# Optimization experiments

Hardware: AMD Instinct MI355X
Metric: run time of the kernel (lower is better)

## Reference

```python
import jax, jax.numpy as jnp
import numpy as np

# Static config matching init_kwargs
T_Q, Q_H, Q_W = 8, 14, 14
T_K, K_H, K_W = 8, 14, 14


def _rel_idx(k_len, q_len):
    # ratios are round(max(ratio, 1.0)) per original code
    q_ratio = round(max(k_len / q_len, 1.0))
    k_ratio = round(max(q_len / k_len, 1.0))
    dist = jnp.arange(k_len)[:, None] * k_ratio - jnp.arange(q_len)[None, :] * q_ratio
    return dist + (q_len - 1) * q_ratio  # [k_len, q_len], values in [0, 2*max_dist]


def setup_inputs() -> dict:
    key = jax.random.key(0)
    k1, k2, k3, k4, k5 = jax.random.split(key, 5)
    B, N, C = 2, 8, 64
    return {
        "key": jax.random.normal(k1, (B, N, T_K, K_H, K_W, C), dtype=jnp.float32),
        "scores": jax.random.normal(k2, (B, N, T_Q * Q_H * Q_W, T_K * K_H * K_W), dtype=jnp.float32),
        "height_embeddings": jax.random.normal(k3, (2 * (max(Q_H, K_H) - 1) + 1, C), dtype=jnp.float32),
        "width_embeddings": jax.random.normal(k4, (2 * (max(Q_W, K_W) - 1) + 1, C), dtype=jnp.float32),
        "time_embeddings": jax.random.normal(k5, (2 * (max(T_Q, T_K) - 1) + 1, C), dtype=jnp.float32),
    }


def reference(key, scores, height_embeddings, width_embeddings, time_embeddings):
    B, N = key.shape[0], key.shape[1]
    # Gather relative-position embeddings: Rh [k_h, q_h, c], Rw [k_w, q_w, c], Rt [T_k, T_q, c]
    Rh = height_embeddings[_rel_idx(K_H, Q_H)]
    Rw = width_embeddings[_rel_idx(K_W, Q_W)]
    Rt = time_embeddings[_rel_idx(T_K, T_Q)]
    # key: [B, N, T_k, k_h, k_w, c]
    rel_h = jnp.einsum('hqc,bnshwc->bnqshw', Rh, key)  # q = q_h
    rel_w = jnp.einsum('wqc,bnshwc->bnqshw', Rw, key)  # q = q_w
    rel_t = jnp.einsum('sqc,bnshwc->bnqshw', Rt, key)  # q = T_q
    s = scores.reshape(B, N, T_Q, Q_H, Q_W, T_K, K_H, K_W)
    s = (s
         + rel_h[:, :, None, :, None, :, :, :]
         + rel_w[:, :, None, None, :, :, :, :]
         + rel_t[:, :, :, None, None, :, :, :])
    return s.reshape(B, N, T_Q * Q_H * Q_W, T_K * K_H * K_W)
```

## Files before the change

### kernel.cpp

```cpp
#include <hip/hip_runtime.h>


typedef float f4 __attribute__((ext_vector_type(4)));

#define BN_TOTAL    16
#define KLEN        1568
#define KLEN4       392
#define QLEN        1568
#define KV_TOTAL    (BN_TOTAL * KLEN)
#define REL_H_ELEMS (BN_TOTAL * 14 * KLEN)
#define REL_T_ELEMS (BN_TOTAL * 8 * KLEN)

#define EROWS  69
#define EPITCH 68

__global__ __launch_bounds__(256) void rel_fused(const float* __restrict__ key,
                                                 const float* __restrict__ hemb,
                                                 const float* __restrict__ wemb,
                                                 const float* __restrict__ temb,
                                                 float* __restrict__ relh,
                                                 float* __restrict__ relw,
                                                 float* __restrict__ relt)
{
    __shared__ float se[EROWS * EPITCH];
    for (int idx = threadIdx.x; idx < EROWS * 64; idx += 256) {
        int row = idx >> 6, c = idx & 63;
        float v;
        if (row < 27)      v = hemb[row * 64 + c];
        else if (row < 54) v = wemb[(row - 27) * 64 + c];
        else               v = temb[(row - 54) * 64 + c];
        se[row * EPITCH + c] = v;
    }
    __syncthreads();

    int tid  = threadIdx.x;
    int s    = tid & 3;
    int kv   = blockIdx.x * 64 + (tid >> 2);
    int bn   = kv / KLEN;
    int k    = kv - bn * KLEN;
    int tk   = k / 196;
    int khw  = k - tk * 196;
    int kh   = khw / 14;
    int kw   = khw - kh * 14;

    f4 kr[16];
    const f4* kp = (const f4*)key + (size_t)kv * 16;
#pragma unroll
    for (int c = 0; c < 16; ++c) kr[c] = kp[c];

#pragma unroll
    for (int j = 0; j < 9; ++j) {
        int qi = s + 4 * j;
        int row = (qi < 14) ? (kh - qi + 13)
                : (qi < 28) ? (kw - qi + 54)
                            : (tk - qi + 89);
        float* dst = (qi < 14) ? relh + (size_t)(bn * 14 + qi) * KLEN
                   : (qi < 28) ? relw + (size_t)(bn * 14 + qi - 14) * KLEN
                               : relt + (size_t)(bn * 8 + qi - 28) * KLEN;
        const f4* e = (const f4*)(se + row * EPITCH);
        f4 acc4 = {0.f, 0.f, 0.f, 0.f};
#pragma unroll
        for (int c = 0; c < 16; ++c) acc4 += kr[c] * e[c];
        dst[k] = acc4.x + acc4.y + acc4.z + acc4.w;
    }
}

#define CH4    56
#define NCH    7
#define SROWS  21
#define STAGE4 (SROWS * CH4)
#define TILE4  (98 * CH4)

__global__ __launch_bounds__(256) void add_staged(const f4* __restrict__ scores,
                                                  const f4* __restrict__ relh,
                                                  const f4* __restrict__ relw,
                                                  const f4* __restrict__ relt,
                                                  f4* __restrict__ out)
{
    __shared__ f4 se[STAGE4];

    int tid = threadIdx.x;
    int b   = blockIdx.x;
    int ch  = b % NCH;  b /= NCH;
    int half = b & 1;   b >>= 1;
    int tq  = b & 7;    b >>= 3;
    int bn  = b;
    int cbase = ch * CH4;

    const f4* wrow = relw + (size_t)(bn * 14) * KLEN4 + cbase;
    const f4* hrow = relh + (size_t)(bn * 14 + half * 7) * KLEN4 + cbase;
    const f4* trow = relt + (size_t)(bn * 8 + tq) * KLEN4 + cbase;

    for (int e = tid; e < STAGE4; e += 256) {
        int r = e / CH4, c = e - r * CH4;
        f4 v;
        if (r < 14) v = wrow[(size_t)r * KLEN4 + c];
        else        v = hrow[(size_t)(r - 14) * KLEN4 + c] + trow[c];
        se[e] = v;
    }

    int obase = (bn * QLEN + tq * 196 + half * 98) * KLEN4 + cbase;

#define EIDX(J, e, row, c, gi)                        \
    int e   = tid + (J) * 256;                        \
    int row = e / CH4;                                \
    int c   = e - row * CH4;                          \
    int gi  = obase + row * KLEN4 + c;

#define LOAD3(G, sv)                                  \
    {                                                 \
        _Pragma("unroll")                             \
        for (int jj = 0; jj < 3; ++jj) {              \
            EIDX(3 * (G) + jj, e, row, c, gi)         \
            sv[jj] = scores[gi];                      \
        }                                             \
    }

#define PROC3(G, sv)                                  \
    {                                                 \
        _Pragma("unroll")                             \
        for (int jj = 0; jj < 3; ++jj) {              \
            EIDX(3 * (G) + jj, e, row, c, gi)         \
            int qhl = row / 14, qw = row - qhl * 14;  \
            f4 v = sv[jj] + se[qw * CH4 + c]          \
                          + se[(14 + qhl) * CH4 + c]; \
            __builtin_nontemporal_store(v, out + gi); \
        }                                             \
    }

    f4 sA[3], sB[3];

    LOAD3(0, sA);
    LOAD3(1, sB);
    __syncthreads();

    PROC3(0, sA);  LOAD3(2, sA);
    PROC3(1, sB);  LOAD3(3, sB);
    PROC3(2, sA);  LOAD3(4, sA);
    PROC3(3, sB);  LOAD3(5, sB);
    PROC3(4, sA);  LOAD3(6, sA);
    PROC3(5, sB);
    PROC3(6, sA);

    if (tid < TILE4 - 21 * 256) {
        EIDX(21, e, row, c, gi)
        int qhl = row / 14, qw = row - qhl * 14;
        f4 v = scores[gi] + se[qw * CH4 + c] + se[(14 + qhl) * CH4 + c];
        __builtin_nontemporal_store(v, out + gi);
    }
#undef EIDX
#undef LOAD3
#undef PROC3
}

extern "C" void kernel_launch(void* const* d_in, const int* in_sizes, int n_in,
                              void* d_out, int out_size, void* d_ws, size_t ws_size,
                              hipStream_t stream)
{
    const float* key    = (const float*)d_in[0];
    const float* scores = (const float*)d_in[1];
    const float* hemb   = (const float*)d_in[2];
    const float* wemb   = (const float*)d_in[3];
    const float* temb   = (const float*)d_in[4];
    float*       out    = (float*)d_out;

    size_t need = (size_t)(REL_H_ELEMS * 2 + REL_T_ELEMS) * sizeof(float);
    if (ws_size < need) return;

    float* relh = (float*)d_ws;
    float* relw = relh + REL_H_ELEMS;
    float* relt = relw + REL_H_ELEMS;

    rel_fused<<<KV_TOTAL * 4 / 256, 256, 0, stream>>>(key, hemb, wemb, temb,
                                                      relh, relw, relt);

    add_staged<<<BN_TOTAL * 8 * 2 * NCH, 256, 0, stream>>>((const f4*)scores,
                                                           (const f4*)relh,
                                                           (const f4*)relw,
                                                           (const f4*)relt,
                                                           (f4*)out);
}
```

Measured before the change: 61.59 us.

## Deepen scores prefetch before staging and split rel kernel across more threads

In the add kernel, eight score vectors per thread are now prefetched into registers before the shared-memory staging of the relative-position rows, rather than six. The staging loads and the barrier therefore overlap with more outstanding global reads, and the remaining groups are software-pipelined across four register buffers. In the rel kernel, each key vector is now handled by 8 threads instead of 4, which doubles the grid and leaves each thread with at most 5 dot products instead of 9. The costs are higher register pressure in the add kernel and redundant key loads in the rel kernel.

Result: no change. 62.57 us (+1.6%).

```diff
diff --git a/kernel.cpp b/kernel.cpp
--- a/kernel.cpp
+++ b/kernel.cpp
@@ -34,8 +34,8 @@
     __syncthreads();
 
     int tid  = threadIdx.x;
-    int s    = tid & 3;
-    int kv   = blockIdx.x * 64 + (tid >> 2);
+    int s    = tid & 7;
+    int kv   = blockIdx.x * 32 + (tid >> 3);
     int bn   = kv / KLEN;
     int k    = kv - bn * KLEN;
     int tk   = k / 196;
@@ -49,19 +49,21 @@
     for (int c = 0; c < 16; ++c) kr[c] = kp[c];
 
 #pragma unroll
-    for (int j = 0; j < 9; ++j) {
-        int qi = s + 4 * j;
-        int row = (qi < 14) ? (kh - qi + 13)
-                : (qi < 28) ? (kw - qi + 54)
-                            : (tk - qi + 89);
-        float* dst = (qi < 14) ? relh + (size_t)(bn * 14 + qi) * KLEN
-                   : (qi < 28) ? relw + (size_t)(bn * 14 + qi - 14) * KLEN
-                               : relt + (size_t)(bn * 8 + qi - 28) * KLEN;
-        const f4* e = (const f4*)(se + row * EPITCH);
-        f4 acc4 = {0.f, 0.f, 0.f, 0.f};
+    for (int j = 0; j < 5; ++j) {
+        int qi = s + 8 * j;
+        if (qi < 36) {
+            int row = (qi < 14) ? (kh - qi + 13)
+                    : (qi < 28) ? (kw - qi + 54)
+                                : (tk - qi + 89);
+            float* dst = (qi < 14) ? relh + (size_t)(bn * 14 + qi) * KLEN
+                       : (qi < 28) ? relw + (size_t)(bn * 14 + qi - 14) * KLEN
+                                   : relt + (size_t)(bn * 8 + qi - 28) * KLEN;
+            const f4* e = (const f4*)(se + row * EPITCH);
+            f4 acc4 = {0.f, 0.f, 0.f, 0.f};
 #pragma unroll
-        for (int c = 0; c < 16; ++c) acc4 += kr[c] * e[c];
-        dst[k] = acc4.x + acc4.y + acc4.z + acc4.w;
+            for (int c = 0; c < 16; ++c) acc4 += kr[c] * e[c];
+            dst[k] = acc4.x + acc4.y + acc4.z + acc4.w;
+        }
     }
 }
 
@@ -87,70 +89,79 @@
     int bn  = b;
     int cbase = ch * CH4;
 
-    const f4* wrow = relw + (size_t)(bn * 14) * KLEN4 + cbase;
-    const f4* hrow = relh + (size_t)(bn * 14 + half * 7) * KLEN4 + cbase;
-    const f4* trow = relt + (size_t)(bn * 8 + tq) * KLEN4 + cbase;
+    int obase = (bn * QLEN + tq * 196 + half * 98) * KLEN4 + cbase;
 
-    for (int e = tid; e < STAGE4; e += 256) {
-        int r = e / CH4, c = e - r * CH4;
-        f4 v;
-        if (r < 14) v = wrow[(size_t)r * KLEN4 + c];
-        else        v = hrow[(size_t)(r - 14) * KLEN4 + c] + trow[c];
-        se[e] = v;
+#define MKIDX(E, row, c, gi)                          \
+    int row = (E) / CH4;                              \
+    int c   = (E) - row * CH4;                        \
+    int gi  = obase + row * KLEN4 + c;
+
+#define LOADG(G, sv)                                              \
+    {                                                             \
+        int eA = (G) * 512 + tid;                                 \
+        MKIDX(eA, rA, cA, giA)                                    \
+        sv[0] = scores[giA];                                      \
+        if ((G) < 10 || tid < 112) {                              \
+            int eB = (G) * 512 + 256 + tid;                       \
+            MKIDX(eB, rB, cB, giB)                                \
+            sv[1] = scores[giB];                                  \
+        }                                                         \
     }
 
-    int obase = (bn * QLEN + tq * 196 + half * 98) * KLEN4 + cbase;
-
-#define EIDX(J, e, row, c, gi)                        \
-    int e   = tid + (J) * 256;                        \
-    int row = e / CH4;                                \
-    int c   = e - row * CH4;                          \
-    int gi  = obase + row * KLEN4 + c;
-
-#define LOAD3(G, sv)                                  \
-    {                                                 \
-        _Pragma("unroll")                             \
-        for (int jj = 0; jj < 3; ++jj) {              \
-            EIDX(3 * (G) + jj, e, row, c, gi)         \
-            sv[jj] = scores[gi];                      \
-        }                                             \
+#define PROCG(G, sv)                                              \
+    {                                                             \
+        int eA = (G) * 512 + tid;                                 \
+        MKIDX(eA, rA, cA, giA)                                    \
+        int qhA = rA / 14, qwA = rA - qhA * 14;                   \
+        f4 vA = sv[0] + se[qwA * CH4 + cA]                        \
+                      + se[(14 + qhA) * CH4 + cA];                \
+        __builtin_nontemporal_store(vA, out + giA);               \
+        if ((G) < 10 || tid < 112) {                              \
+            int eB = (G) * 512 + 256 + tid;                       \
+            MKIDX(eB, rB, cB, giB)                                \
+            int qhB = rB / 14, qwB = rB - qhB * 14;               \
+            f4 vB = sv[1] + se[qwB * CH4 + cB]                    \
+                          + se[(14 + qhB) * CH4 + cB];            \
+            __builtin_nontemporal_store(vB, out + giB);           \
+        }                                                         \
     }
 
-#define PROC3(G, sv)                                  \
-    {                                                 \
-        _Pragma("unroll")                             \
-        for (int jj = 0; jj < 3; ++jj) {              \
-            EIDX(3 * (G) + jj, e, row, c, gi)         \
-            int qhl = row / 14, qw = row - qhl * 14;  \
-            f4 v = sv[jj] + se[qw * CH4 + c]          \
-                          + se[(14 + qhl) * CH4 + c]; \
-            __builtin_nontemporal_store(v, out + gi); \
-        }                                             \
+    f4 s0[2], s1[2], s2[2], s3[2];
+
+    LOADG(0, s0);
+    LOADG(1, s1);
+    LOADG(2, s2);
+    LOADG(3, s3);
+
+    {
+        const f4* wrow = relw + (size_t)(bn * 14) * KLEN4 + cbase;
+        const f4* hrow = relh + (size_t)(bn * 14 + half * 7) * KLEN4 + cbase;
+        const f4* trow = relt + (size_t)(bn * 8 + tq) * KLEN4 + cbase;
+        for (int e = tid; e < STAGE4; e += 256) {
+            int r = e / CH4, c = e - r * CH4;
+            f4 v;
+            if (r < 14) v = wrow[(size_t)r * KLEN4 + c];
+            else        v = hrow[(size_t)(r - 14) * KLEN4 + c] + trow[c];
+            se[e] = v;
+        }
     }
-
-    f4 sA[3], sB[3];
-
-    LOAD3(0, sA);
-    LOAD3(1, sB);
     __syncthreads();
 
-    PROC3(0, sA);  LOAD3(2, sA);
-    PROC3(1, sB);  LOAD3(3, sB);
-    PROC3(2, sA);  LOAD3(4, sA);
-    PROC3(3, sB);  LOAD3(5, sB);
-    PROC3(4, sA);  LOAD3(6, sA);
-    PROC3(5, sB);
-    PROC3(6, sA);
+    PROCG(0, s0);  LOADG(4, s0);
+    PROCG(1, s1);  LOADG(5, s1);
+    PROCG(2, s2);  LOADG(6, s2);
+    PROCG(3, s3);  LOADG(7, s3);
+    PROCG(4, s0);  LOADG(8, s0);
+    PROCG(5, s1);  LOADG(9, s1);
+    PROCG(6, s2);  LOADG(10, s2);
+    PROCG(7, s3);
+    PROCG(8, s0);
+    PROCG(9, s1);
+    PROCG(10, s2);
 
-    if (tid < TILE4 - 21 * 256) {
-        EIDX(21, e, row, c, gi)
-        int qhl = row / 14, qw = row - qhl * 14;
-        f4 v = scores[gi] + se[qw * CH4 + c] + se[(14 + qhl) * CH4 + c];
-        __builtin_nontemporal_store(v, out + gi);
-    }
-#undef EIDX
-#undef LOAD3
-#undef PROC3
+#undef MKIDX
+#undef LOADG
+#undef PROCG
 }
 
 extern "C" void kernel_launch(void* const* d_in, const int* in_sizes, int n_in,
@@ -171,7 +182,7 @@
     float* relw = relh + REL_H_ELEMS;
     float* relt = relw + REL_H_ELEMS;
 
-    rel_fused<<<KV_TOTAL * 4 / 256, 256, 0, stream>>>(key, hemb, wemb, temb,
+    rel_fused<<<KV_TOTAL * 8 / 256, 256, 0, stream>>>(key, hemb, wemb, temb,
                                                       relh, relw, relt);
 
     add_staged<<<BN_TOTAL * 8 * 2 * NCH, 256, 0, stream>>>((const f4*)scores,
```
